# Kernel optimization log

Measured on AMD Instinct MI355X. Metric: run time of the kernel, lower is better.

The kernel has to match this reference:

```python
import jax, jax.numpy as jnp
import numpy as np

ROUTINGS = 3

def squash(v):
    # v: [..., D]
    n = jnp.linalg.norm(v, axis=-1, keepdims=True)
    n2 = n * n
    return (n2 / (1.0 + n2)) * v / (n + 1e-8)

def setup_inputs() -> dict:
    key = jax.random.key(0)
    k1, k2 = jax.random.split(key)
    B, O, I, D_out, D_in = 64, 32, 512, 64, 64
    x = jax.random.normal(k1, (B, I, D_in), dtype=jnp.float32)
    # xavier_uniform with gain=1.141 over last two dims (out_dim, in_dim)
    fan_in, fan_out = D_in, D_out
    bound = 1.141 * np.sqrt(6.0 / (fan_in + fan_out))
    weight = jax.random.uniform(k2, (O, I, D_out, D_in), dtype=jnp.float32,
                                minval=-bound, maxval=bound)
    return {"x": x, "weight": weight}

def reference(x, weight):
    # x: [B, I, D_in]; weight: [O, I, D_out, D_in]
    B = x.shape[0]
    O, I = weight.shape[0], weight.shape[1]
    # x_hat[b,o,i,d] = sum_m W[o,i,d,m] x[b,i,m]  -> [B, O, I, D_out]
    x_hat = jnp.einsum('oidm,bim->boid', weight, x)
    x_hat_detach = jax.lax.stop_gradient(x_hat)
    b = jnp.zeros((B, O, I), dtype=x.dtype)
    out = None
    for i in range(ROUTINGS):
        c = jax.nn.softmax(b, axis=1)  # softmax over out_num
        if i == ROUTINGS - 1:
            out = squash(jnp.einsum('boi,boid->bod', c, x_hat))
        else:
            out = squash(jnp.einsum('boi,boid->bod', c, x_hat_detach))
            # agreement: [B,O,I,D] . [B,O,D] -> [B,O,I]
            b = b + jnp.einsum('boid,bod->boi', x_hat_detach, out)
    return out  # [B, O, D_out]
```

## Files before the change

kernel.cpp:

```cpp
#include <hip/hip_runtime.h>
#include <stdint.h>

#define NB 64
#define NO 32
#define NI 512
#define ND 64

typedef __attribute__((ext_vector_type(8))) short short8;
typedef __attribute__((ext_vector_type(4))) float f32x4;

__device__ __forceinline__ float blo(unsigned int u) {
    union { unsigned int i; float f; } v; v.i = u << 16; return v.f;
}
__device__ __forceinline__ float bhi(unsigned int u) {
    union { unsigned int i; float f; } v; v.i = u & 0xFFFF0000u; return v.f;
}
__device__ __forceinline__ unsigned short f2bf(float f) {
    union { float f; unsigned int i; } v; v.f = f;
    return (unsigned short)((v.i + 0x7FFFu + ((v.i >> 16) & 1u)) >> 16);
}
__device__ __forceinline__ short8 pack8(const float4 a, const float4 b) {
    short8 r;
    r[0] = (short)f2bf(a.x); r[1] = (short)f2bf(a.y);
    r[2] = (short)f2bf(a.z); r[3] = (short)f2bf(a.w);
    r[4] = (short)f2bf(b.x); r[5] = (short)f2bf(b.y);
    r[6] = (short)f2bf(b.z); r[7] = (short)f2bf(b.w);
    return r;
}

__global__ __launch_bounds__(256) void k_gemm(const float* __restrict__ x,
                                              const float* __restrict__ w,
                                              unsigned short* __restrict__ xh) {
    const int o  = blockIdx.x & 31;
    const int ig = blockIdx.x >> 5;
    const int t  = threadIdx.x;
    const int wv = t >> 6;
    const int l  = t & 63;
    const int q  = l >> 4;
    const int c  = l & 15;

    for (int ii = 0; ii < 8; ++ii) {
        const int i = ig * 8 + ii;
        const float* ap = x + ((size_t)(16 * wv + c) * NI + i) * 64 + q * 8;
        const short8 a0 = pack8(*(const float4*)ap,        *(const float4*)(ap + 4));
        const short8 a1 = pack8(*(const float4*)(ap + 32), *(const float4*)(ap + 36));
        const size_t wbase = ((size_t)o * NI + i) * 64 * 64;
        f32x4 acc[4];
        #pragma unroll
        for (int td = 0; td < 4; ++td) {
            const float* bp = w + wbase + (size_t)(16 * td + c) * 64 + q * 8;
            const short8 b0 = pack8(*(const float4*)bp,        *(const float4*)(bp + 4));
            const short8 b1 = pack8(*(const float4*)(bp + 32), *(const float4*)(bp + 36));
            f32x4 z = {0.f, 0.f, 0.f, 0.f};
            z = __builtin_amdgcn_mfma_f32_16x16x32_bf16(a0, b0, z, 0, 0, 0);
            z = __builtin_amdgcn_mfma_f32_16x16x32_bf16(a1, b1, z, 0, 0, 0);
            acc[td] = z;
        }
        #pragma unroll
        for (int td = 0; td < 4; ++td) {
            const int d = 16 * td + c;
            #pragma unroll
            for (int r = 0; r < 4; ++r) {
                const int b = 16 * wv + 4 * q + r;
                xh[(((size_t)o * NB + b) * NI + i) * ND + d] = f2bf(acc[td][r]);
            }
        }
    }
}

template<int STEP>
__global__ __launch_bounds__(256) void k_route(const unsigned short* __restrict__ xh,
                                               const float* __restrict__ b_in,
                                               float* __restrict__ b_out,
                                               float* __restrict__ outp) {
    constexpr int XS = 68;
    extern __shared__ char smem[];
    unsigned short* xh_s = (unsigned short*)smem;
    float* c_s = (float*)(smem + 69632);
    float* P   = (float*)(smem + 69632 + 2048);
    float* o_s = (float*)(smem + 69632 + 2048 + 1024);

    const int t = threadIdx.x;
    const int b = blockIdx.x >> 5;
    const int o = blockIdx.x & 31;

    float b_own0 = 0.f, b_own1 = 0.f;
    if (STEP > 0) {
        const float* bp = b_in + (size_t)b * (NO * NI);
        #pragma unroll
        for (int s = 0; s < 2; ++s) {
            const int i = t + s * 256;
            float v[NO];
            #pragma unroll
            for (int oo = 0; oo < NO; ++oo) v[oo] = bp[(size_t)oo * NI + i];
            float m = v[0];
            #pragma unroll
            for (int oo = 1; oo < NO; ++oo) m = fmaxf(m, v[oo]);
            float Z = 0.f;
            #pragma unroll
            for (int oo = 0; oo < NO; ++oo) Z += __expf(v[oo] - m);
            const float own = bp[(size_t)o * NI + i];
            c_s[i] = __expf(own - m) / Z;
            if (s == 0) b_own0 = own; else b_own1 = own;
        }
        __syncthreads();
    }

    const int dg = t & 7;
    const int ip = t >> 3;
    const unsigned short* gsrc = xh + ((size_t)o * NB + b) * NI * ND;
    float acc[8] = {0, 0, 0, 0, 0, 0, 0, 0};
    #pragma unroll
    for (int k = 0; k < 16; ++k) {
        const int i = 32 * k + ip;
        const uint4 raw = *(const uint4*)(gsrc + (size_t)i * ND + dg * 8);
        unsigned short* dst = xh_s + i * XS + dg * 8;
        *(uint2*)dst = make_uint2(raw.x, raw.y);
        *(uint2*)(dst + 4) = make_uint2(raw.z, raw.w);
        const float cw = (STEP == 0) ? 0.03125f : c_s[i];
        acc[0] += cw * blo(raw.x); acc[1] += cw * bhi(raw.x);
        acc[2] += cw * blo(raw.y); acc[3] += cw * bhi(raw.y);
        acc[4] += cw * blo(raw.z); acc[5] += cw * bhi(raw.z);
        acc[6] += cw * blo(raw.w); acc[7] += cw * bhi(raw.w);
    }
    #pragma unroll
    for (int j = 0; j < 8; ++j) {
        acc[j] += __shfl_xor(acc[j], 8);
        acc[j] += __shfl_xor(acc[j], 16);
        acc[j] += __shfl_xor(acc[j], 32);
    }
    const int lane = t & 63;
    const int wv = t >> 6;
    if (lane < 8) {
        #pragma unroll
        for (int j = 0; j < 8; ++j) P[wv * 64 + lane * 8 + j] = acc[j];
    }
    __syncthreads();

    if (t < 64) {
        const float sv = P[t] + P[64 + t] + P[128 + t] + P[192 + t];
        float s2 = sv * sv;
        #pragma unroll
        for (int m = 1; m < 64; m <<= 1) s2 += __shfl_xor(s2, m);
        const float n = sqrtf(s2);
        const float sc = (s2 / (1.0f + s2)) / (n + 1e-8f);
        const float ov = sv * sc;
        o_s[t] = ov;
        if (STEP == 2) outp[((size_t)b * NO + o) * ND + t] = ov;
    }
    __syncthreads();

    if (STEP < 2) {
        #pragma unroll
        for (int s = 0; s < 2; ++s) {
            const int i = t + s * 256;
            const unsigned short* row = xh_s + i * XS;
            float dot = 0.f;
            #pragma unroll
            for (int cc = 0; cc < 8; ++cc) {
                const uint2 ra = *(const uint2*)(row + cc * 8);
                const uint2 rb = *(const uint2*)(row + cc * 8 + 4);
                const float* oc = o_s + cc * 8;
                dot += blo(ra.x) * oc[0] + bhi(ra.x) * oc[1]
                     + blo(ra.y) * oc[2] + bhi(ra.y) * oc[3]
                     + blo(rb.x) * oc[4] + bhi(rb.x) * oc[5]
                     + blo(rb.y) * oc[6] + bhi(rb.y) * oc[7];
            }
            b_out[((size_t)b * NO + o) * NI + i] = (s == 0 ? b_own0 : b_own1) + dot;
        }
    }
}

extern "C" void kernel_launch(void* const* d_in, const int* in_sizes, int n_in,
                              void* d_out, int out_size, void* d_ws, size_t ws_size,
                              hipStream_t stream) {
    const float* x = (const float*)d_in[0];
    const float* w = (const float*)d_in[1];
    float* outp = (float*)d_out;

    char* ws = (char*)d_ws;
    unsigned short* xh = (unsigned short*)ws;
    float* ba = (float*)(ws + (size_t)134217728);
    float* bb = (float*)(ws + (size_t)134217728 + 4194304);

    const int smem = 69632 + 2048 + 1024 + 256;
    hipFuncSetAttribute(reinterpret_cast<const void*>(&k_route<0>),
                        hipFuncAttributeMaxDynamicSharedMemorySize, smem);
    hipFuncSetAttribute(reinterpret_cast<const void*>(&k_route<1>),
                        hipFuncAttributeMaxDynamicSharedMemorySize, smem);
    hipFuncSetAttribute(reinterpret_cast<const void*>(&k_route<2>),
                        hipFuncAttributeMaxDynamicSharedMemorySize, smem);

    k_gemm<<<dim3(2048), dim3(256), 0, stream>>>(x, w, xh);
    k_route<0><<<dim3(2048), dim3(256), smem, stream>>>(xh, nullptr, ba, nullptr);
    k_route<1><<<dim3(2048), dim3(256), smem, stream>>>(xh, ba, bb, nullptr);
    k_route<2><<<dim3(2048), dim3(256), smem, stream>>>(xh, bb, nullptr, outp);
}
```

Before: 550.4 us.

## Keep routing tiles in registers, drop big LDS staging, prefetch GEMM operands

The routing kernel now holds each thread's x_hat slice in registers instead of copying it into a 68KB shared-memory tile, and computes the agreement dot product with warp shuffles. This frees LDS so more blocks fit per CU. The softmax becomes a single-pass online max/sum over O. The GEMM kernel software-prefetches the next i's x and weight fragments into registers while the current one is processed. Both changes raise register pressure, which could cut occupancy or cause spills.

```diff
diff --git a/kernel.cpp b/kernel.cpp
--- a/kernel.cpp
+++ b/kernel.cpp
@@ -26,6 +26,22 @@
     r[4] = (short)f2bf(b.x); r[5] = (short)f2bf(b.y);
     r[6] = (short)f2bf(b.z); r[7] = (short)f2bf(b.w);
     return r;
+}
+
+__device__ __forceinline__ void ld_a(float4 r[4], const float* __restrict__ p) {
+    r[0] = *(const float4*)(p);
+    r[1] = *(const float4*)(p + 4);
+    r[2] = *(const float4*)(p + 32);
+    r[3] = *(const float4*)(p + 36);
+}
+__device__ __forceinline__ void ld_b(float4 r[16], const float* __restrict__ p) {
+    #pragma unroll
+    for (int td = 0; td < 4; ++td) {
+        r[4 * td + 0] = *(const float4*)(p + td * 1024);
+        r[4 * td + 1] = *(const float4*)(p + td * 1024 + 4);
+        r[4 * td + 2] = *(const float4*)(p + td * 1024 + 32);
+        r[4 * td + 3] = *(const float4*)(p + td * 1024 + 36);
+    }
 }
 
 __global__ __launch_bounds__(256) void k_gemm(const float* __restrict__ x,
@@ -39,18 +55,27 @@
     const int q  = l >> 4;
     const int c  = l & 15;
 
+    const float* ap0 = x + ((size_t)(16 * wv + c) * NI + ig * 8) * 64 + q * 8;
+    const float* bp0 = w + ((size_t)o * NI + ig * 8) * 4096 + (size_t)c * 64 + q * 8;
+
+    float4 ra[4], rb[16], na[4], nb[16];
+    ld_a(ra, ap0);
+    ld_b(rb, bp0);
+
+    #pragma unroll
     for (int ii = 0; ii < 8; ++ii) {
+        if (ii < 7) {
+            ld_a(na, ap0 + (ii + 1) * 64);
+            ld_b(nb, bp0 + (size_t)(ii + 1) * 4096);
+        }
         const int i = ig * 8 + ii;
-        const float* ap = x + ((size_t)(16 * wv + c) * NI + i) * 64 + q * 8;
-        const short8 a0 = pack8(*(const float4*)ap,        *(const float4*)(ap + 4));
-        const short8 a1 = pack8(*(const float4*)(ap + 32), *(const float4*)(ap + 36));
-        const size_t wbase = ((size_t)o * NI + i) * 64 * 64;
+        const short8 a0 = pack8(ra[0], ra[1]);
+        const short8 a1 = pack8(ra[2], ra[3]);
         f32x4 acc[4];
         #pragma unroll
         for (int td = 0; td < 4; ++td) {
-            const float* bp = w + wbase + (size_t)(16 * td + c) * 64 + q * 8;
-            const short8 b0 = pack8(*(const float4*)bp,        *(const float4*)(bp + 4));
-            const short8 b1 = pack8(*(const float4*)(bp + 32), *(const float4*)(bp + 36));
+            const short8 b0 = pack8(rb[4 * td + 0], rb[4 * td + 1]);
+            const short8 b1 = pack8(rb[4 * td + 2], rb[4 * td + 3]);
             f32x4 z = {0.f, 0.f, 0.f, 0.f};
             z = __builtin_amdgcn_mfma_f32_16x16x32_bf16(a0, b0, z, 0, 0, 0);
             z = __builtin_amdgcn_mfma_f32_16x16x32_bf16(a1, b1, z, 0, 0, 0);
@@ -65,6 +90,10 @@
                 xh[(((size_t)o * NB + b) * NI + i) * ND + d] = f2bf(acc[td][r]);
             }
         }
+        #pragma unroll
+        for (int j = 0; j < 4; ++j)  ra[j] = na[j];
+        #pragma unroll
+        for (int j = 0; j < 16; ++j) rb[j] = nb[j];
     }
 }
 
@@ -73,55 +102,48 @@
                                                const float* __restrict__ b_in,
                                                float* __restrict__ b_out,
                                                float* __restrict__ outp) {
-    constexpr int XS = 68;
-    extern __shared__ char smem[];
-    unsigned short* xh_s = (unsigned short*)smem;
-    float* c_s = (float*)(smem + 69632);
-    float* P   = (float*)(smem + 69632 + 2048);
-    float* o_s = (float*)(smem + 69632 + 2048 + 1024);
-
-    const int t = threadIdx.x;
-    const int b = blockIdx.x >> 5;
-    const int o = blockIdx.x & 31;
-
-    float b_own0 = 0.f, b_own1 = 0.f;
+    __shared__ float c_s[NI];
+    __shared__ float P[4 * 64];
+    __shared__ float o_s[64];
+
+    const int t  = threadIdx.x;
+    const int b  = blockIdx.x >> 5;
+    const int o  = blockIdx.x & 31;
+    const int dg = t & 7;
+    const int ip = t >> 3;
+
+    const unsigned short* gsrc = xh + ((size_t)o * NB + b) * NI * ND;
+    uint4 raw[16];
+    #pragma unroll
+    for (int k = 0; k < 16; ++k)
+        raw[k] = *(const uint4*)(gsrc + (size_t)(32 * k + ip) * ND + dg * 8);
+
+    const float* bp = (STEP > 0) ? (b_in + (size_t)b * (NO * NI)) : nullptr;
     if (STEP > 0) {
-        const float* bp = b_in + (size_t)b * (NO * NI);
         #pragma unroll
         for (int s = 0; s < 2; ++s) {
             const int i = t + s * 256;
-            float v[NO];
+            float m = -INFINITY, Z = 0.f;
             #pragma unroll
-            for (int oo = 0; oo < NO; ++oo) v[oo] = bp[(size_t)oo * NI + i];
-            float m = v[0];
-            #pragma unroll
-            for (int oo = 1; oo < NO; ++oo) m = fmaxf(m, v[oo]);
-            float Z = 0.f;
-            #pragma unroll
-            for (int oo = 0; oo < NO; ++oo) Z += __expf(v[oo] - m);
-            const float own = bp[(size_t)o * NI + i];
-            c_s[i] = __expf(own - m) / Z;
-            if (s == 0) b_own0 = own; else b_own1 = own;
+            for (int oo = 0; oo < NO; ++oo) {
+                const float v = bp[(size_t)oo * NI + i];
+                const float nm = fmaxf(m, v);
+                Z = Z * __expf(m - nm) + __expf(v - nm);
+                m = nm;
+            }
+            c_s[i] = __expf(bp[(size_t)o * NI + i] - m) / Z;
         }
         __syncthreads();
     }
 
-    const int dg = t & 7;
-    const int ip = t >> 3;
-    const unsigned short* gsrc = xh + ((size_t)o * NB + b) * NI * ND;
     float acc[8] = {0, 0, 0, 0, 0, 0, 0, 0};
     #pragma unroll
     for (int k = 0; k < 16; ++k) {
-        const int i = 32 * k + ip;
-        const uint4 raw = *(const uint4*)(gsrc + (size_t)i * ND + dg * 8);
-        unsigned short* dst = xh_s + i * XS + dg * 8;
-        *(uint2*)dst = make_uint2(raw.x, raw.y);
-        *(uint2*)(dst + 4) = make_uint2(raw.z, raw.w);
-        const float cw = (STEP == 0) ? 0.03125f : c_s[i];
-        acc[0] += cw * blo(raw.x); acc[1] += cw * bhi(raw.x);
-        acc[2] += cw * blo(raw.y); acc[3] += cw * bhi(raw.y);
-        acc[4] += cw * blo(raw.z); acc[5] += cw * bhi(raw.z);
-        acc[6] += cw * blo(raw.w); acc[7] += cw * bhi(raw.w);
+        const float cw = (STEP == 0) ? 0.03125f : c_s[32 * k + ip];
+        acc[0] += cw * blo(raw[k].x); acc[1] += cw * bhi(raw[k].x);
+        acc[2] += cw * blo(raw[k].y); acc[3] += cw * bhi(raw[k].y);
+        acc[4] += cw * blo(raw[k].z); acc[5] += cw * bhi(raw[k].z);
+        acc[6] += cw * blo(raw[k].w); acc[7] += cw * bhi(raw[k].w);
     }
     #pragma unroll
     for (int j = 0; j < 8; ++j) {
@@ -151,23 +173,29 @@
     __syncthreads();
 
     if (STEP < 2) {
-        #pragma unroll
-        for (int s = 0; s < 2; ++s) {
-            const int i = t + s * 256;
-            const unsigned short* row = xh_s + i * XS;
-            float dot = 0.f;
-            #pragma unroll
-            for (int cc = 0; cc < 8; ++cc) {
-                const uint2 ra = *(const uint2*)(row + cc * 8);
-                const uint2 rb = *(const uint2*)(row + cc * 8 + 4);
-                const float* oc = o_s + cc * 8;
-                dot += blo(ra.x) * oc[0] + bhi(ra.x) * oc[1]
-                     + blo(ra.y) * oc[2] + bhi(ra.y) * oc[3]
-                     + blo(rb.x) * oc[4] + bhi(rb.x) * oc[5]
-                     + blo(rb.y) * oc[6] + bhi(rb.y) * oc[7];
-            }
-            b_out[((size_t)b * NO + o) * NI + i] = (s == 0 ? b_own0 : b_own1) + dot;
-        }
+        float oc[8];
+        #pragma unroll
+        for (int j = 0; j < 8; ++j) oc[j] = o_s[dg * 8 + j];
+        float w1 = 0.f, w2 = 0.f;
+        #pragma unroll
+        for (int k = 0; k < 16; ++k) {
+            float pd = blo(raw[k].x) * oc[0] + bhi(raw[k].x) * oc[1]
+                     + blo(raw[k].y) * oc[2] + bhi(raw[k].y) * oc[3]
+                     + blo(raw[k].z) * oc[4] + bhi(raw[k].z) * oc[5]
+                     + blo(raw[k].w) * oc[6] + bhi(raw[k].w) * oc[7];
+            pd += __shfl_xor(pd, 1);
+            pd += __shfl_xor(pd, 2);
+            pd += __shfl_xor(pd, 4);
+            if (k == dg)     w1 = pd;
+            if (k == dg + 8) w2 = pd;
+        }
+        const int i1 = 32 * dg + ip;
+        const int i2 = 32 * (dg + 8) + ip;
+        float* bo = b_out + ((size_t)b * NO + o) * NI;
+        const float own1 = (STEP == 0) ? 0.f : bp[(size_t)o * NI + i1];
+        const float own2 = (STEP == 0) ? 0.f : bp[(size_t)o * NI + i2];
+        bo[i1] = own1 + w1;
+        bo[i2] = own2 + w2;
     }
 }
 
@@ -183,16 +211,8 @@
     float* ba = (float*)(ws + (size_t)134217728);
     float* bb = (float*)(ws + (size_t)134217728 + 4194304);
 
-    const int smem = 69632 + 2048 + 1024 + 256;
-    hipFuncSetAttribute(reinterpret_cast<const void*>(&k_route<0>),
-                        hipFuncAttributeMaxDynamicSharedMemorySize, smem);
-    hipFuncSetAttribute(reinterpret_cast<const void*>(&k_route<1>),
-                        hipFuncAttributeMaxDynamicSharedMemorySize, smem);
-    hipFuncSetAttribute(reinterpret_cast<const void*>(&k_route<2>),
-                        hipFuncAttributeMaxDynamicSharedMemorySize, smem);
-
     k_gemm<<<dim3(2048), dim3(256), 0, stream>>>(x, w, xh);
-    k_route<0><<<dim3(2048), dim3(256), smem, stream>>>(xh, nullptr, ba, nullptr);
-    k_route<1><<<dim3(2048), dim3(256), smem, stream>>>(xh, ba, bb, nullptr);
-    k_route<2><<<dim3(2048), dim3(256), smem, stream>>>(xh, bb, nullptr, outp);
-}
+    k_route<0><<<dim3(2048), dim3(256), 0, stream>>>(xh, nullptr, ba, nullptr);
+    k_route<1><<<dim3(2048), dim3(256), 0, stream>>>(xh, ba, bb, nullptr);
+    k_route<2><<<dim3(2048), dim3(256), 0, stream>>>(xh, bb, nullptr, outp);
+}
```

New measurement: 530.5 us. -3.6%, faster.
